# Kernel optimization log

Hardware: AMD Instinct MI355X
Metric: run time of the kernel (lower is better)

## Reference

```python
import jax, jax.numpy as jnp
import numpy as np

N_NODES = 50000
N_EDGES = 600000
D_IN = 128
D_OUT = 128
LN_EPS = 1e-5


def setup_inputs() -> dict:
    key = jax.random.key(0)
    ks = jax.random.split(key, 12)
    x = jax.random.normal(ks[0], (N_NODES, D_IN), dtype=jnp.float32)
    adj_in_rows = jax.random.randint(ks[1], (N_EDGES,), 0, N_NODES, dtype=jnp.int32)
    adj_in_cols = jax.random.randint(ks[2], (N_EDGES,), 0, N_NODES, dtype=jnp.int32)
    adj_in_vals = jax.random.uniform(ks[3], (N_EDGES,), dtype=jnp.float32)
    adj_out_rows = jax.random.randint(ks[4], (N_EDGES,), 0, N_NODES, dtype=jnp.int32)
    adj_out_cols = jax.random.randint(ks[5], (N_EDGES,), 0, N_NODES, dtype=jnp.int32)
    adj_out_vals = jax.random.uniform(ks[6], (N_EDGES,), dtype=jnp.float32)
    s = 1.0 / np.sqrt(D_IN)
    W_self = jax.random.uniform(ks[7], (D_OUT, D_IN), dtype=jnp.float32, minval=-s, maxval=s)
    b_self = jax.random.uniform(ks[8], (D_OUT,), dtype=jnp.float32, minval=-s, maxval=s)
    W_in = jax.random.uniform(ks[9], (D_OUT, D_IN), dtype=jnp.float32, minval=-s, maxval=s)
    W_out = jax.random.uniform(ks[10], (D_OUT, D_IN), dtype=jnp.float32, minval=-s, maxval=s)
    ln_gamma = jnp.ones((D_OUT,), dtype=jnp.float32)
    ln_beta = jnp.zeros((D_OUT,), dtype=jnp.float32)
    return {
        "x": x,
        "adj_in_rows": adj_in_rows, "adj_in_cols": adj_in_cols, "adj_in_vals": adj_in_vals,
        "adj_out_rows": adj_out_rows, "adj_out_cols": adj_out_cols, "adj_out_vals": adj_out_vals,
        "W_self": W_self, "b_self": b_self, "W_in": W_in, "W_out": W_out,
        "ln_gamma": ln_gamma, "ln_beta": ln_beta,
    }


def _spmm(rows, cols, vals, x, n):
    # COO sparse.mm: out[r] += vals[e] * x[cols[e]]
    return jax.ops.segment_sum(vals[:, None] * x[cols], rows, num_segments=n)


def reference(x, adj_in_rows, adj_in_cols, adj_in_vals,
              adj_out_rows, adj_out_cols, adj_out_vals,
              W_self, b_self, W_in, W_out, ln_gamma, ln_beta):
    n = x.shape[0]
    agg_in = _spmm(adj_in_rows, adj_in_cols, adj_in_vals, x, n)
    agg_out = _spmm(adj_out_rows, adj_out_cols, adj_out_vals, x, n)
    h = x @ W_self.T + b_self + agg_in @ W_in.T + agg_out @ W_out.T
    mu = jnp.mean(h, axis=-1, keepdims=True)
    var = jnp.mean(jnp.square(h - mu), axis=-1, keepdims=True)
    h = (h - mu) * jax.lax.rsqrt(var + LN_EPS) * ln_gamma + ln_beta
    # dropout is identity in eval mode (training=False)
    return jax.nn.relu(h)
```

## Files before the change

kernel.cpp:

```cpp
#include <hip/hip_runtime.h>

#define N_NODES 50000
#define N_EDGES 600000
#define D 128
#define BM 32
#define NT (2 * N_NODES)
#define NE2 (2 * N_EDGES)
#define NPAD 50048
#define KA 384
#define GBM 64
#define NB 1563
#define BROWS 64
#define CAPE 1024
#define CHUNK_A 8192

typedef __attribute__((ext_vector_type(8))) short bf16x8;
typedef __attribute__((ext_vector_type(4))) float f32x4;

__device__ inline unsigned short bfr(float x) {
    unsigned b = __float_as_uint(x);
    b += 0x7FFFu + ((b >> 16) & 1u);
    return (unsigned short)(b >> 16);
}
__device__ inline float bf_lo(unsigned u) { return __uint_as_float(u << 16); }
__device__ inline float bf_hi(unsigned u) { return __uint_as_float(u & 0xFFFF0000u); }


__global__ __launch_bounds__(256) void cvt_x(const float* __restrict__ x, short* __restrict__ A)
{
    int gid = blockIdx.x * 256 + threadIdx.x;
    if (gid >= N_NODES * 32) return;
    int row = gid >> 5, c4 = gid & 31;
    float4 v = *reinterpret_cast<const float4*>(x + (size_t)row * D + c4 * 4);
    ushort4 o = { bfr(v.x), bfr(v.y), bfr(v.z), bfr(v.w) };
    *reinterpret_cast<ushort4*>(A + (size_t)row * KA + c4 * 4) = o;
}

__global__ __launch_bounds__(384) void cvt_w(
    const float* __restrict__ Ws, const float* __restrict__ Wi,
    const float* __restrict__ Wo, short* __restrict__ Wc)
{
    int j = blockIdx.x, k = threadIdx.x;
    float v = (k < 128) ? Ws[j * 128 + k]
            : (k < 256) ? Wi[j * 128 + k - 128]
                        : Wo[j * 128 + k - 256];
    Wc[j * KA + k] = (short)bfr(v);
}


__global__ __launch_bounds__(1024) void bucket_hist(
    const int* __restrict__ ir, const int* __restrict__ orow, int* __restrict__ bcnt)
{
    __shared__ int h[NB];
    for (int i = threadIdx.x; i < NB; i += 1024) h[i] = 0;
    __syncthreads();
    int stride = gridDim.x * 1024;
    for (int e = blockIdx.x * 1024 + threadIdx.x; e < NE2; e += stride) {
        int r = (e < N_EDGES) ? ir[e] : N_NODES + orow[e - N_EDGES];
        atomicAdd(&h[r >> 6], 1);
    }
    __syncthreads();
    for (int i = threadIdx.x; i < NB; i += 1024)
        if (h[i]) atomicAdd(&bcnt[i], h[i]);
}

__global__ __launch_bounds__(1024) void scan_buckets(
    const int* __restrict__ bcnt, int* __restrict__ bbase, int* __restrict__ bcur)
{
    __shared__ int s[1024];
    const int t = threadIdx.x;
    const int i0 = 2 * t, i1 = 2 * t + 1;
    int v0 = (i0 < NB) ? bcnt[i0] : 0;
    int v1 = (i1 < NB) ? bcnt[i1] : 0;
    int v = v0 + v1;
    s[t] = v;
    __syncthreads();
    for (int o = 1; o < 1024; o <<= 1) {
        int u = (t >= o) ? s[t - o] : 0;
        __syncthreads();
        s[t] += u;
        __syncthreads();
    }
    int ex = s[t] - v;
    if (i0 < NB) { bbase[i0] = ex;      bcur[i0] = ex; }
    if (i1 < NB) { bbase[i1] = ex + v0; bcur[i1] = ex + v0; }
}

__global__ __launch_bounds__(1024) void scatter_buckets(
    const int* __restrict__ ir, const int* __restrict__ icol, const float* __restrict__ ival,
    const int* __restrict__ orow, const int* __restrict__ ocol, const float* __restrict__ oval,
    int* __restrict__ bcur, int2* __restrict__ pairp)
{
    __shared__ int2 pay[CHUNK_A];
    __shared__ int  dstp[CHUNK_A];
    __shared__ int  hist[NB];
    __shared__ int  lofs[NB];
    __shared__ int  gb2[NB];
    __shared__ int  sbuf[1024];

    const int t = threadIdx.x;
    for (int i = t; i < NB; i += 1024) hist[i] = 0;
    __syncthreads();

    const int e0 = blockIdx.x * CHUNK_A;
    const int m = min(NE2 - e0, CHUNK_A);
    int rr[8], cc[8]; float vv[8];
#pragma unroll
    for (int i = 0; i < 8; ++i) {
        int e = e0 + t + i * 1024;
        if (e < N_EDGES)      { rr[i] = ir[e];                       cc[i] = icol[e];           vv[i] = ival[e]; }
        else if (e < NE2)     { rr[i] = N_NODES + orow[e - N_EDGES]; cc[i] = ocol[e - N_EDGES]; vv[i] = oval[e - N_EDGES]; }
        else                  { rr[i] = -1; cc[i] = 0; vv[i] = 0.f; }
        if (rr[i] >= 0) atomicAdd(&hist[rr[i] >> 6], 1);
    }
    __syncthreads();

    const int i0 = 2 * t, i1 = 2 * t + 1;
    int h0 = (i0 < NB) ? hist[i0] : 0;
    int h1 = (i1 < NB) ? hist[i1] : 0;
    int hv = h0 + h1;
    sbuf[t] = hv;
    __syncthreads();
    for (int o = 1; o < 1024; o <<= 1) {
        int u = (t >= o) ? sbuf[t - o] : 0;
        __syncthreads();
        sbuf[t] += u;
        __syncthreads();
    }
    int ex = sbuf[t] - hv;
    if (i0 < NB) lofs[i0] = ex;
    if (i1 < NB) lofs[i1] = ex + h0;
    __syncthreads();

    for (int i = t; i < NB; i += 1024) {
        int c = hist[i];
        int g = c ? atomicAdd(&bcur[i], c) : 0;
        gb2[i] = g - lofs[i];
    }
    __syncthreads();
    for (int i = t; i < NB; i += 1024) hist[i] = lofs[i];
    __syncthreads();

#pragma unroll
    for (int i = 0; i < 8; ++i) {
        if (rr[i] < 0) continue;
        int bk = rr[i] >> 6;
        int s = atomicAdd(&hist[bk], 1);
        pay[s]  = make_int2((cc[i] & 0xFFFF) | ((rr[i] & 63) << 16), __float_as_int(vv[i]));
        dstp[s] = gb2[bk] + s;
    }
    __syncthreads();

    for (int i = t; i < m; i += 1024)
        pairp[dstp[i]] = pay[i];
}

__global__ __launch_bounds__(512) void bucket_spmm(
    const int* __restrict__ bbase, const int* __restrict__ bcnt,
    const int2* __restrict__ pairp, short* __restrict__ A)
{
    __shared__ int2 ed[CAPE];
    __shared__ int  rs[BROWS];
    __shared__ int  rstart[BROWS + 1];
    __shared__ int  rcur[BROWS];

    const int t = threadIdx.x;
    const int b = blockIdx.x;
    const int base = bbase[b];
    const int n = bcnt[b];
    const int w = t >> 6, lane = t & 63;
    const int h = lane >> 5, sl = lane & 31;
    const int row0 = w * 8;
    const char* Ab = (const char*)A + sl * 8;

    float4 acc[8];
#pragma unroll
    for (int i = 0; i < 8; ++i) acc[i] = make_float4(0.f, 0.f, 0.f, 0.f);

    for (int s0 = 0; s0 < n; s0 += CAPE) {
        const int m = min(n - s0, CAPE);
        if (t < BROWS) rs[t] = 0;
        __syncthreads();
        int2 myp[2];
#pragma unroll
        for (int k = 0; k < 2; ++k) {
            int i = t + k * 512;
            if (i < m) {
                myp[k] = pairp[base + s0 + i];
                atomicAdd(&rs[(myp[k].x >> 16) & 63], 1);
            }
        }
        __syncthreads();
        if (t < 64) {
            int v = rs[t];
            int a = v;
#pragma unroll
            for (int o = 1; o < 64; o <<= 1) {
                int u = __shfl_up(a, o);
                if (t >= o) a += u;
            }
            rstart[t] = a - v;
            rcur[t]   = a - v;
            if (t == 63) rstart[64] = a;
        }
        __syncthreads();
#pragma unroll
        for (int k = 0; k < 2; ++k) {
            int i = t + k * 512;
            if (i < m) {
                int pos = atomicAdd(&rcur[(myp[k].x >> 16) & 63], 1);
                ed[pos] = myp[k];
            }
        }
        __syncthreads();
#pragma unroll
        for (int ri = 0; ri < 8; ++ri) {
            const int r = row0 + ri;
            const int s = rstart[r], e2 = rstart[r + 1];
            float4 a = acc[ri];
            for (int i = s; i < e2; i += 8) {
#pragma unroll
                for (int k = 0; k < 4; ++k) {
                    int idx = i + 2 * k + h;
                    int2 p = ed[min(idx, e2 - 1)];
                    float v = (idx < e2) ? __int_as_float(p.y) : 0.f;
                    uint2 u = *(const uint2*)(Ab + (unsigned)((p.x & 0xFFFF) * (KA * 2)));
                    a.x += v * bf_lo(u.x);
                    a.y += v * bf_hi(u.x);
                    a.z += v * bf_lo(u.y);
                    a.w += v * bf_hi(u.y);
                }
            }
            acc[ri] = a;
        }
        __syncthreads();
    }

    char* Aw = (char*)A;
#pragma unroll
    for (int ri = 0; ri < 8; ++ri) {
        float4 a = acc[ri];
        a.x += __shfl_xor(a.x, 32);
        a.y += __shfl_xor(a.y, 32);
        a.z += __shfl_xor(a.z, 32);
        a.w += __shfl_xor(a.w, 32);
        int wv = b * BROWS + row0 + ri;
        if (lane < 32 && wv < NT) {
            uint2 o;
            o.x = ((unsigned)bfr(a.y) << 16) | (unsigned)bfr(a.x);
            o.y = ((unsigned)bfr(a.w) << 16) | (unsigned)bfr(a.z);
            size_t dst = (wv < N_NODES)
                       ? ((size_t)wv * (KA * 2) + 256 + sl * 8)
                       : ((size_t)(wv - N_NODES) * (KA * 2) + 512 + sl * 8);
            *(uint2*)(Aw + dst) = o;
        }
    }
}

__global__ __launch_bounds__(512) void gemm_mfma(
    const short* __restrict__ A, const short* __restrict__ Wc,
    const float* __restrict__ b, const float* __restrict__ gamma,
    const float* __restrict__ beta, float* __restrict__ out)
{
    __shared__ short Alds[GBM * KA];
    __shared__ float red[8][64][2];
    __shared__ float2 mustd[64];

    const int t = threadIdx.x;
    const int l = t & 63, w = t >> 6;
    const int q = l >> 4, c = l & 15;
    const int base = blockIdx.x * GBM;

    bf16x8 bfrag[12];
    const short* wrow = Wc + (size_t)(w * 16 + c) * KA + q * 8;
#pragma unroll
    for (int s = 0; s < 12; ++s)
        bfrag[s] = *reinterpret_cast<const bf16x8*>(wrow + s * 32);

#pragma unroll
    for (int i = 0; i < 6; ++i) {
        int slot = t + i * 512;
        int row = slot / 48, c16 = slot % 48;
        bf16x8 v = *reinterpret_cast<const bf16x8*>(A + (size_t)(base + row) * KA + c16 * 8);
        *reinterpret_cast<bf16x8*>(&Alds[row * KA + (c16 ^ (row & 7)) * 8]) = v;
    }
    __syncthreads();

    f32x4 acc[4];
#pragma unroll
    for (int rg = 0; rg < 4; ++rg) acc[rg] = (f32x4){0.f, 0.f, 0.f, 0.f};

#pragma unroll
    for (int s = 0; s < 12; ++s) {
#pragma unroll
        for (int rg = 0; rg < 4; ++rg) {
            int row = rg * 16 + c;
            int c16 = (s * 4 + q) ^ (row & 7);
            bf16x8 af = *reinterpret_cast<const bf16x8*>(&Alds[row * KA + c16 * 8]);
            acc[rg] = __builtin_amdgcn_mfma_f32_16x16x32_bf16(af, bfrag[s], acc[rg], 0, 0, 0);
        }
    }

    const float bj = b[w * 16 + c];
    const float gj = gamma[w * 16 + c];
    const float ej = beta[w * 16 + c];

#pragma unroll
    for (int rg = 0; rg < 4; ++rg) {
#pragma unroll
        for (int r = 0; r < 4; ++r) {
            float hv = acc[rg][r] + bj;
            acc[rg][r] = hv;
            float s1 = hv, s2 = hv * hv;
#pragma unroll
            for (int m = 1; m < 16; m <<= 1) {
                s1 += __shfl_xor(s1, m);
                s2 += __shfl_xor(s2, m);
            }
            if (c == 0) {
                int row = rg * 16 + q * 4 + r;
                red[w][row][0] = s1;
                red[w][row][1] = s2;
            }
        }
    }
    __syncthreads();

    if (t < 64) {
        float s1 = 0.f, s2 = 0.f;
#pragma unroll
        for (int ww = 0; ww < 8; ++ww) { s1 += red[ww][t][0]; s2 += red[ww][t][1]; }
        float mu = s1 * (1.f / 128.f);
        float var = s2 * (1.f / 128.f) - mu * mu;
        mustd[t] = make_float2(mu, rsqrtf(var + 1e-5f));
    }
    __syncthreads();

#pragma unroll
    for (int rg = 0; rg < 4; ++rg) {
        int row0 = rg * 16 + q * 4;
        int node0 = base + row0;
#pragma unroll
        for (int r = 0; r < 4; ++r) {
            float2 ms = mustd[row0 + r];
            float y = (acc[rg][r] - ms.x) * ms.y * gj + ej;
            y = fmaxf(y, 0.f);
            if (node0 + r < N_NODES)
                out[(size_t)(node0 + r) * D + w * 16 + c] = y;
        }
    }
}

__global__ __launch_bounds__(256) void spmm_scatter(
    const int* __restrict__ rows, const int* __restrict__ cols,
    const float* __restrict__ vals, const float* __restrict__ x,
    float* __restrict__ agg, int nE)
{
    int g = blockIdx.x * 256 + threadIdx.x;
    int e = g >> 5;
    if (e >= nE) return;
    int q = g & 31;
    int r = rows[e], c = cols[e];
    float v = vals[e];
    float4 xv = *reinterpret_cast<const float4*>(x + (size_t)c * D + (size_t)q * 4);
    float* ap = agg + (size_t)r * D + (size_t)q * 4;
    atomicAdd(ap + 0, v * xv.x);
    atomicAdd(ap + 1, v * xv.y);
    atomicAdd(ap + 2, v * xv.z);
    atomicAdd(ap + 3, v * xv.w);
}

__global__ __launch_bounds__(256) void gemm_ln_relu(
    const float* __restrict__ x, const float* __restrict__ agg_in,
    const float* __restrict__ agg_out,
    const float* __restrict__ Ws, const float* __restrict__ Wi,
    const float* __restrict__ Wo, const float* __restrict__ b,
    const float* __restrict__ gamma, const float* __restrict__ beta,
    float* __restrict__ out, int n)
{
    __shared__ float4 Wl[D * (D / 4)];
    __shared__ float4 Xl[BM * (D / 4)];

    const int t = threadIdx.x;
    const int l = t & 63;
    const int w = t >> 6;
    const int base = blockIdx.x * BM;
    const int j0 = l, j1 = l + 64;

    float acc0[8], acc1[8];
    const float bj0 = b[j0], bj1 = b[j1];
#pragma unroll
    for (int i = 0; i < 8; ++i) { acc0[i] = bj0; acc1[i] = bj1; }

    const float* srcs[3] = { x, agg_in, agg_out };
    const float* wms[3]  = { Ws, Wi, Wo };

#pragma unroll
    for (int s = 0; s < 3; ++s) {
        const float4* src4 = reinterpret_cast<const float4*>(srcs[s]);
        const float4* w4   = reinterpret_cast<const float4*>(wms[s]);
        __syncthreads();
#pragma unroll
        for (int it = 0; it < 16; ++it) {
            int gi = t + 256 * it;
            int j = gi >> 5, k4 = gi & 31;
            Wl[j * 32 + (k4 ^ (j & 7))] = w4[gi];
        }
#pragma unroll
        for (int it = 0; it < 4; ++it) {
            int gi = t + 256 * it;
            int m = gi >> 5, k4 = gi & 31;
            int node = base + m;
            float4 v = (node < n) ? src4[(size_t)node * 32 + k4]
                                  : make_float4(0.f, 0.f, 0.f, 0.f);
            Xl[m * 32 + k4] = v;
        }
        __syncthreads();

        const int sw = j0 & 7;
#pragma unroll 8
        for (int k4 = 0; k4 < 32; ++k4) {
            float4 w0 = Wl[j0 * 32 + (k4 ^ sw)];
            float4 w1 = Wl[j1 * 32 + (k4 ^ sw)];
#pragma unroll
            for (int i = 0; i < 8; ++i) {
                float4 xv = Xl[(w + 4 * i) * 32 + k4];
                acc0[i] += xv.x * w0.x + xv.y * w0.y + xv.z * w0.z + xv.w * w0.w;
                acc1[i] += xv.x * w1.x + xv.y * w1.y + xv.z * w1.z + xv.w * w1.w;
            }
        }
    }

    const float g0 = gamma[j0], g1 = gamma[j1];
    const float be0 = beta[j0], be1 = beta[j1];
#pragma unroll
    for (int i = 0; i < 8; ++i) {
        int node = base + w + 4 * i;
        float s  = acc0[i] + acc1[i];
        float ss = acc0[i] * acc0[i] + acc1[i] * acc1[i];
#pragma unroll
        for (int off = 32; off; off >>= 1) {
            s  += __shfl_xor(s, off);
            ss += __shfl_xor(ss, off);
        }
        float mu   = s * (1.0f / D);
        float var  = ss * (1.0f / D) - mu * mu;
        float rstd = rsqrtf(var + 1e-5f);
        if (node < n) {
            float y0 = (acc0[i] - mu) * rstd * g0 + be0;
            float y1 = (acc1[i] - mu) * rstd * g1 + be1;
            out[(size_t)node * D + j0] = fmaxf(y0, 0.f);
            out[(size_t)node * D + j1] = fmaxf(y1, 0.f);
        }
    }
}

extern "C" void kernel_launch(void* const* d_in, const int* in_sizes, int n_in,
                              void* d_out, int out_size, void* d_ws, size_t ws_size,
                              hipStream_t stream) {
    const float* x     = (const float*)d_in[0];
    const int*   ir    = (const int*)  d_in[1];
    const int*   icoln = (const int*)  d_in[2];
    const float* ival  = (const float*)d_in[3];
    const int*   orow  = (const int*)  d_in[4];
    const int*   ocol  = (const int*)  d_in[5];
    const float* oval  = (const float*)d_in[6];
    const float* Ws    = (const float*)d_in[7];
    const float* b     = (const float*)d_in[8];
    const float* Wi    = (const float*)d_in[9];
    const float* Wo    = (const float*)d_in[10];
    const float* gamma = (const float*)d_in[11];
    const float* beta  = (const float*)d_in[12];
    float* out = (float*)d_out;

    short* A     = (short*)d_ws;
    short* Wc    = A + (size_t)NPAD * KA;
    int*   bcnt  = (int*)(Wc + (size_t)128 * KA);
    int*   bbase = bcnt + NB;
    int*   bcur  = bbase + NB;
    int2*  pairp = (int2*)(bcur + NB + ((3 * NB) & 1));
    size_t need  = (size_t)NPAD * KA * 2 + (size_t)128 * KA * 2
                 + (size_t)(3 * NB + 2) * 4 + (size_t)NE2 * 8;

    if (ws_size >= need) {
        hipMemsetAsync(bcnt, 0, NB * sizeof(int), stream);
        hipMemsetAsync(A + (size_t)N_NODES * KA, 0,
                       (size_t)(NPAD - N_NODES) * KA * 2, stream);

        cvt_x<<<(N_NODES * 32 + 255) / 256, 256, 0, stream>>>(x, A);
        cvt_w<<<128, 384, 0, stream>>>(Ws, Wi, Wo, Wc);

        bucket_hist<<<128, 1024, 0, stream>>>(ir, orow, bcnt);
        scan_buckets<<<1, 1024, 0, stream>>>(bcnt, bbase, bcur);
        scatter_buckets<<<(NE2 + CHUNK_A - 1) / CHUNK_A, 1024, 0, stream>>>(
            ir, icoln, ival, orow, ocol, oval, bcur, pairp);
        bucket_spmm<<<NB, 512, 0, stream>>>(bbase, bcnt, pairp, A);

        gemm_mfma<<<NPAD / GBM, 512, 0, stream>>>(A, Wc, b, gamma, beta, out);
    } else {
        float* agg_in  = (float*)d_ws;
        float* agg_out = agg_in + (size_t)N_NODES * D;
        hipMemsetAsync(d_ws, 0, 2 * (size_t)N_NODES * D * sizeof(float), stream);
        const int eblocks = (N_EDGES * 32 + 255) / 256;
        spmm_scatter<<<eblocks, 256, 0, stream>>>(ir, icoln, ival, x, agg_in, N_EDGES);
        spmm_scatter<<<eblocks, 256, 0, stream>>>(orow, ocol, oval, x, agg_out, N_EDGES);
        const int gblocks = (N_NODES + BM - 1) / BM;
        gemm_ln_relu<<<gblocks, 256, 0, stream>>>(x, agg_in, agg_out, Ws, Wi, Wo,
                                                  b, gamma, beta, out, N_NODES);
    }
}
```

Measured before the change: 137.9 us.

## Fuse bucketed SpMM aggregation into MFMA GEMM with per-node buckets

```diff
diff --git a/kernel.cpp b/kernel.cpp
--- a/kernel.cpp
+++ b/kernel.cpp
@@ -8,9 +8,8 @@
 #define NE2 (2 * N_EDGES)
 #define NPAD 50048
 #define KA 384
-#define GBM 64
-#define NB 1563
-#define BROWS 64
+#define NBK 782
+#define VR 128
 #define CAPE 1024
 #define CHUNK_A 8192
 
@@ -26,14 +25,14 @@
 __device__ inline float bf_hi(unsigned u) { return __uint_as_float(u & 0xFFFF0000u); }
 
 
-__global__ __launch_bounds__(256) void cvt_x(const float* __restrict__ x, short* __restrict__ A)
+__global__ __launch_bounds__(256) void cvt_x(const float* __restrict__ x, short* __restrict__ Xb)
 {
     int gid = blockIdx.x * 256 + threadIdx.x;
     if (gid >= N_NODES * 32) return;
     int row = gid >> 5, c4 = gid & 31;
     float4 v = *reinterpret_cast<const float4*>(x + (size_t)row * D + c4 * 4);
     ushort4 o = { bfr(v.x), bfr(v.y), bfr(v.z), bfr(v.w) };
-    *reinterpret_cast<ushort4*>(A + (size_t)row * KA + c4 * 4) = o;
+    *reinterpret_cast<ushort4*>(Xb + (size_t)row * D + c4 * 4) = o;
 }
 
 __global__ __launch_bounds__(384) void cvt_w(
@@ -51,16 +50,16 @@
 __global__ __launch_bounds__(1024) void bucket_hist(
     const int* __restrict__ ir, const int* __restrict__ orow, int* __restrict__ bcnt)
 {
-    __shared__ int h[NB];
-    for (int i = threadIdx.x; i < NB; i += 1024) h[i] = 0;
+    __shared__ int h[NBK];
+    for (int i = threadIdx.x; i < NBK; i += 1024) h[i] = 0;
     __syncthreads();
     int stride = gridDim.x * 1024;
     for (int e = blockIdx.x * 1024 + threadIdx.x; e < NE2; e += stride) {
-        int r = (e < N_EDGES) ? ir[e] : N_NODES + orow[e - N_EDGES];
-        atomicAdd(&h[r >> 6], 1);
-    }
-    __syncthreads();
-    for (int i = threadIdx.x; i < NB; i += 1024)
+        int node = (e < N_EDGES) ? ir[e] : orow[e - N_EDGES];
+        atomicAdd(&h[node >> 6], 1);
+    }
+    __syncthreads();
+    for (int i = threadIdx.x; i < NBK; i += 1024)
         if (h[i]) atomicAdd(&bcnt[i], h[i]);
 }
 
@@ -69,10 +68,7 @@
 {
     __shared__ int s[1024];
     const int t = threadIdx.x;
-    const int i0 = 2 * t, i1 = 2 * t + 1;
-    int v0 = (i0 < NB) ? bcnt[i0] : 0;
-    int v1 = (i1 < NB) ? bcnt[i1] : 0;
-    int v = v0 + v1;
+    int v = (t < NBK) ? bcnt[t] : 0;
     s[t] = v;
     __syncthreads();
     for (int o = 1; o < 1024; o <<= 1) {
@@ -81,9 +77,7 @@
         s[t] += u;
         __syncthreads();
     }
-    int ex = s[t] - v;
-    if (i0 < NB) { bbase[i0] = ex;      bcur[i0] = ex; }
-    if (i1 < NB) { bbase[i1] = ex + v0; bcur[i1] = ex + v0; }
+    if (t < NBK) { bbase[t] = s[t] - v; bcur[t] = s[t] - v; }
 }
 
 __global__ __launch_bounds__(1024) void scatter_buckets(
@@ -93,32 +87,35 @@
 {
     __shared__ int2 pay[CHUNK_A];
     __shared__ int  dstp[CHUNK_A];
-    __shared__ int  hist[NB];
-    __shared__ int  lofs[NB];
-    __shared__ int  gb2[NB];
+    __shared__ int  hist[NBK];
+    __shared__ int  lofs[NBK];
+    __shared__ int  gb2[NBK];
     __shared__ int  sbuf[1024];
 
     const int t = threadIdx.x;
-    for (int i = t; i < NB; i += 1024) hist[i] = 0;
+    for (int i = t; i < NBK; i += 1024) hist[i] = 0;
     __syncthreads();
 
     const int e0 = blockIdx.x * CHUNK_A;
     const int m = min(NE2 - e0, CHUNK_A);
-    int rr[8], cc[8]; float vv[8];
+    int bk8[8], px[8], vv[8];
 #pragma unroll
     for (int i = 0; i < 8; ++i) {
         int e = e0 + t + i * 1024;
-        if (e < N_EDGES)      { rr[i] = ir[e];                       cc[i] = icol[e];           vv[i] = ival[e]; }
-        else if (e < NE2)     { rr[i] = N_NODES + orow[e - N_EDGES]; cc[i] = ocol[e - N_EDGES]; vv[i] = oval[e - N_EDGES]; }
-        else                  { rr[i] = -1; cc[i] = 0; vv[i] = 0.f; }
-        if (rr[i] >= 0) atomicAdd(&hist[rr[i] >> 6], 1);
-    }
-    __syncthreads();
-
-    const int i0 = 2 * t, i1 = 2 * t + 1;
-    int h0 = (i0 < NB) ? hist[i0] : 0;
-    int h1 = (i1 < NB) ? hist[i1] : 0;
-    int hv = h0 + h1;
+        int node, col, flag; float val;
+        if (e < N_EDGES)      { node = ir[e];            col = icol[e];            val = ival[e];            flag = 0; }
+        else if (e < NE2)     { node = orow[e - N_EDGES]; col = ocol[e - N_EDGES]; val = oval[e - N_EDGES];  flag = 64; }
+        else                  { node = -1; col = 0; val = 0.f; flag = 0; }
+        if (node >= 0) {
+            bk8[i] = node >> 6;
+            px[i]  = (col & 0xFFFF) | (((node & 63) | flag) << 16);
+            vv[i]  = __float_as_int(val);
+            atomicAdd(&hist[bk8[i]], 1);
+        } else bk8[i] = -1;
+    }
+    __syncthreads();
+
+    int hv = (t < NBK) ? hist[t] : 0;
     sbuf[t] = hv;
     __syncthreads();
     for (int o = 1; o < 1024; o <<= 1) {
@@ -127,27 +124,24 @@
         sbuf[t] += u;
         __syncthreads();
     }
-    int ex = sbuf[t] - hv;
-    if (i0 < NB) lofs[i0] = ex;
-    if (i1 < NB) lofs[i1] = ex + h0;
-    __syncthreads();
-
-    for (int i = t; i < NB; i += 1024) {
+    if (t < NBK) lofs[t] = sbuf[t] - hv;
+    __syncthreads();
+
+    for (int i = t; i < NBK; i += 1024) {
         int c = hist[i];
         int g = c ? atomicAdd(&bcur[i], c) : 0;
         gb2[i] = g - lofs[i];
     }
     __syncthreads();
-    for (int i = t; i < NB; i += 1024) hist[i] = lofs[i];
+    for (int i = t; i < NBK; i += 1024) hist[i] = lofs[i];
     __syncthreads();
 
 #pragma unroll
     for (int i = 0; i < 8; ++i) {
-        if (rr[i] < 0) continue;
-        int bk = rr[i] >> 6;
-        int s = atomicAdd(&hist[bk], 1);
-        pay[s]  = make_int2((cc[i] & 0xFFFF) | ((rr[i] & 63) << 16), __float_as_int(vv[i]));
-        dstp[s] = gb2[bk] + s;
+        if (bk8[i] < 0) continue;
+        int s = atomicAdd(&hist[bk8[i]], 1);
+        pay[s]  = make_int2(px[i], vv[i]);
+        dstp[s] = gb2[bk8[i]] + s;
     }
     __syncthreads();
 
@@ -155,31 +149,46 @@
         pairp[dstp[i]] = pay[i];
 }
 
-__global__ __launch_bounds__(512) void bucket_spmm(
+__global__ __launch_bounds__(512, 4) void spmm_gemm(
     const int* __restrict__ bbase, const int* __restrict__ bcnt,
-    const int2* __restrict__ pairp, short* __restrict__ A)
-{
-    __shared__ int2 ed[CAPE];
-    __shared__ int  rs[BROWS];
-    __shared__ int  rstart[BROWS + 1];
-    __shared__ int  rcur[BROWS];
+    const int2* __restrict__ pairp, const short* __restrict__ Xb,
+    const short* __restrict__ Wc, const float* __restrict__ b,
+    const float* __restrict__ gamma, const float* __restrict__ beta,
+    float* __restrict__ out)
+{
+    __shared__ short Alds[64 * KA];
+    __shared__ int2  ed[CAPE];
+    __shared__ int   rs[VR];
+    __shared__ int   rstart[VR + 1];
+    __shared__ int   rcur[VR];
+    __shared__ float red[8][64][2];
+    __shared__ float2 mustd[64];
 
     const int t = threadIdx.x;
-    const int b = blockIdx.x;
-    const int base = bbase[b];
-    const int n = bcnt[b];
-    const int w = t >> 6, lane = t & 63;
+    const int bk = blockIdx.x;
+    const int lane = t & 63, w = t >> 6;
     const int h = lane >> 5, sl = lane & 31;
-    const int row0 = w * 8;
-    const char* Ab = (const char*)A + sl * 8;
-
-    float4 acc[8];
-#pragma unroll
-    for (int i = 0; i < 8; ++i) acc[i] = make_float4(0.f, 0.f, 0.f, 0.f);
+    const int nodebase = bk * 64;
+
+#pragma unroll
+    for (int i = 0; i < 2; ++i) {
+        int slot = t + i * 512;
+        int row = slot >> 4, c16 = slot & 15;
+        bf16x8 v = *reinterpret_cast<const bf16x8*>(Xb + (size_t)(nodebase + row) * D + c16 * 8);
+        *reinterpret_cast<bf16x8*>(&Alds[row * KA + (c16 ^ (row & 7)) * 8]) = v;
+    }
+
+    const int base = bbase[bk];
+    const int n = bcnt[bk];
+    const char* Ab = (const char*)Xb + sl * 8;
+
+    float4 acc[16];
+#pragma unroll
+    for (int i = 0; i < 16; ++i) acc[i] = make_float4(0.f, 0.f, 0.f, 0.f);
 
     for (int s0 = 0; s0 < n; s0 += CAPE) {
         const int m = min(n - s0, CAPE);
-        if (t < BROWS) rs[t] = 0;
+        if (t < VR) rs[t] = 0;
         __syncthreads();
         int2 myp[2];
 #pragma unroll
@@ -187,44 +196,45 @@
             int i = t + k * 512;
             if (i < m) {
                 myp[k] = pairp[base + s0 + i];
-                atomicAdd(&rs[(myp[k].x >> 16) & 63], 1);
+                atomicAdd(&rs[(myp[k].x >> 16) & 127], 1);
             }
         }
         __syncthreads();
         if (t < 64) {
-            int v = rs[t];
-            int a = v;
+            int v0 = rs[2 * t], v1 = rs[2 * t + 1];
+            int v = v0 + v1, a = v;
 #pragma unroll
             for (int o = 1; o < 64; o <<= 1) {
                 int u = __shfl_up(a, o);
                 if (t >= o) a += u;
             }
-            rstart[t] = a - v;
-            rcur[t]   = a - v;
-            if (t == 63) rstart[64] = a;
+            int ex = a - v;
+            rstart[2 * t] = ex;          rcur[2 * t] = ex;
+            rstart[2 * t + 1] = ex + v0; rcur[2 * t + 1] = ex + v0;
+            if (t == 63) rstart[VR] = a;
         }
         __syncthreads();
 #pragma unroll
         for (int k = 0; k < 2; ++k) {
             int i = t + k * 512;
             if (i < m) {
-                int pos = atomicAdd(&rcur[(myp[k].x >> 16) & 63], 1);
+                int pos = atomicAdd(&rcur[(myp[k].x >> 16) & 127], 1);
                 ed[pos] = myp[k];
             }
         }
         __syncthreads();
 #pragma unroll
-        for (int ri = 0; ri < 8; ++ri) {
-            const int r = row0 + ri;
+        for (int ri = 0; ri < 16; ++ri) {
+            const int r = w * 16 + ri;
             const int s = rstart[r], e2 = rstart[r + 1];
             float4 a = acc[ri];
-            for (int i = s; i < e2; i += 8) {
-#pragma unroll
-                for (int k = 0; k < 4; ++k) {
+            for (int i = s; i < e2; i += 16) {
+#pragma unroll
+                for (int k = 0; k < 8; ++k) {
                     int idx = i + 2 * k + h;
                     int2 p = ed[min(idx, e2 - 1)];
                     float v = (idx < e2) ? __int_as_float(p.y) : 0.f;
-                    uint2 u = *(const uint2*)(Ab + (unsigned)((p.x & 0xFFFF) * (KA * 2)));
+                    uint2 u = *(const uint2*)(Ab + (unsigned)((p.x & 0xFFFF) * (D * 2)));
                     a.x += v * bf_lo(u.x);
                     a.y += v * bf_hi(u.x);
                     a.z += v * bf_lo(u.y);
@@ -236,68 +246,60 @@
         __syncthreads();
     }
 
-    char* Aw = (char*)A;
-#pragma unroll
-    for (int ri = 0; ri < 8; ++ri) {
+#pragma unroll
+    for (int ri = 0; ri < 16; ++ri) {
         float4 a = acc[ri];
         a.x += __shfl_xor(a.x, 32);
         a.y += __shfl_xor(a.y, 32);
         a.z += __shfl_xor(a.z, 32);
         a.w += __shfl_xor(a.w, 32);
-        int wv = b * BROWS + row0 + ri;
-        if (lane < 32 && wv < NT) {
+        if (lane < 32) {
+            int vrow = w * 16 + ri;
+            int row = vrow & 63;
+            int flag = vrow >> 6;
+            int c16 = 16 + flag * 16 + (sl >> 1);
             uint2 o;
             o.x = ((unsigned)bfr(a.y) << 16) | (unsigned)bfr(a.x);
             o.y = ((unsigned)bfr(a.w) << 16) | (unsigned)bfr(a.z);
-            size_t dst = (wv < N_NODES)
-                       ? ((size_t)wv * (KA * 2) + 256 + sl * 8)
-                       : ((size_t)(wv - N_NODES) * (KA * 2) + 512 + sl * 8);
-            *(uint2*)(Aw + dst) = o;
-        }
-    }
-}
-
-__global__ __launch_bounds__(512) void gemm_mfma(
-    const short* __restrict__ A, const short* __restrict__ Wc,
-    const float* __restrict__ b, const float* __restrict__ gamma,
-    const float* __restrict__ beta, float* __restrict__ out)
-{
-    __shared__ short Alds[GBM * KA];
-    __shared__ float red[8][64][2];
-    __shared__ float2 mustd[64];
-
-    const int t = threadIdx.x;
-    const int l = t & 63, w = t >> 6;
-    const int q = l >> 4, c = l & 15;
-    const int base = blockIdx.x * GBM;
-
-    bf16x8 bfrag[12];
+            char* dst = (char*)Alds + row * (KA * 2) + (c16 ^ (row & 7)) * 16 + (sl & 1) * 8;
+            *(uint2*)dst = o;
+        }
+    }
+
+    const int q = lane >> 4, c = lane & 15;
     const short* wrow = Wc + (size_t)(w * 16 + c) * KA + q * 8;
-#pragma unroll
-    for (int s = 0; s < 12; ++s)
+
+    bf16x8 bfrag[6];
+#pragma unroll
+    for (int s = 0; s < 6; ++s)
         bfrag[s] = *reinterpret_cast<const bf16x8*>(wrow + s * 32);
-
-#pragma unroll
-    for (int i = 0; i < 6; ++i) {
-        int slot = t + i * 512;
-        int row = slot / 48, c16 = slot % 48;
-        bf16x8 v = *reinterpret_cast<const bf16x8*>(A + (size_t)(base + row) * KA + c16 * 8);
-        *reinterpret_cast<bf16x8*>(&Alds[row * KA + (c16 ^ (row & 7)) * 8]) = v;
-    }
-    __syncthreads();
-
-    f32x4 acc[4];
-#pragma unroll
-    for (int rg = 0; rg < 4; ++rg) acc[rg] = (f32x4){0.f, 0.f, 0.f, 0.f};
-
-#pragma unroll
-    for (int s = 0; s < 12; ++s) {
+    __syncthreads();
+
+    f32x4 acg[4];
+#pragma unroll
+    for (int rg = 0; rg < 4; ++rg) acg[rg] = (f32x4){0.f, 0.f, 0.f, 0.f};
+
+#pragma unroll
+    for (int s = 0; s < 6; ++s) {
 #pragma unroll
         for (int rg = 0; rg < 4; ++rg) {
             int row = rg * 16 + c;
             int c16 = (s * 4 + q) ^ (row & 7);
             bf16x8 af = *reinterpret_cast<const bf16x8*>(&Alds[row * KA + c16 * 8]);
-            acc[rg] = __builtin_amdgcn_mfma_f32_16x16x32_bf16(af, bfrag[s], acc[rg], 0, 0, 0);
+            acg[rg] = __builtin_amdgcn_mfma_f32_16x16x32_bf16(af, bfrag[s], acg[rg], 0, 0, 0);
+        }
+    }
+#pragma unroll
+    for (int s = 0; s < 6; ++s)
+        bfrag[s] = *reinterpret_cast<const bf16x8*>(wrow + (s + 6) * 32);
+#pragma unroll
+    for (int s = 0; s < 6; ++s) {
+#pragma unroll
+        for (int rg = 0; rg < 4; ++rg) {
+            int row = rg * 16 + c;
+            int c16 = ((s + 6) * 4 + q) ^ (row & 7);
+            bf16x8 af = *reinterpret_cast<const bf16x8*>(&Alds[row * KA + c16 * 8]);
+            acg[rg] = __builtin_amdgcn_mfma_f32_16x16x32_bf16(af, bfrag[s], acg[rg], 0, 0, 0);
         }
     }
 
@@ -309,13 +311,13 @@
     for (int rg = 0; rg < 4; ++rg) {
 #pragma unroll
         for (int r = 0; r < 4; ++r) {
-            float hv = acc[rg][r] + bj;
-            acc[rg][r] = hv;
+            float hv = acg[rg][r] + bj;
+            acg[rg][r] = hv;
             float s1 = hv, s2 = hv * hv;
 #pragma unroll
-            for (int m = 1; m < 16; m <<= 1) {
-                s1 += __shfl_xor(s1, m);
-                s2 += __shfl_xor(s2, m);
+            for (int m2 = 1; m2 < 16; m2 <<= 1) {
+                s1 += __shfl_xor(s1, m2);
+                s2 += __shfl_xor(s2, m2);
             }
             if (c == 0) {
                 int row = rg * 16 + q * 4 + r;
@@ -339,11 +341,11 @@
 #pragma unroll
     for (int rg = 0; rg < 4; ++rg) {
         int row0 = rg * 16 + q * 4;
-        int node0 = base + row0;
+        int node0 = nodebase + row0;
 #pragma unroll
         for (int r = 0; r < 4; ++r) {
             float2 ms = mustd[row0 + r];
-            float y = (acc[rg][r] - ms.x) * ms.y * gj + ej;
+            float y = (acg[rg][r] - ms.x) * ms.y * gj + ej;
             y = fmaxf(y, 0.f);
             if (node0 + r < N_NODES)
                 out[(size_t)(node0 + r) * D + w * 16 + c] = y;
@@ -473,30 +475,30 @@
     const float* beta  = (const float*)d_in[12];
     float* out = (float*)d_out;
 
-    short* A     = (short*)d_ws;
-    short* Wc    = A + (size_t)NPAD * KA;
+    short* Xb    = (short*)d_ws;
+    short* Wc    = Xb + (size_t)NPAD * D;
     int*   bcnt  = (int*)(Wc + (size_t)128 * KA);
-    int*   bbase = bcnt + NB;
-    int*   bcur  = bbase + NB;
-    int2*  pairp = (int2*)(bcur + NB + ((3 * NB) & 1));
-    size_t need  = (size_t)NPAD * KA * 2 + (size_t)128 * KA * 2
-                 + (size_t)(3 * NB + 2) * 4 + (size_t)NE2 * 8;
+    int*   bbase = bcnt + NBK;
+    int*   bcur  = bbase + NBK;
+    int2*  pairp = (int2*)(bcur + NBK + ((3 * NBK) & 1));
+    size_t need  = (size_t)NPAD * D * 2 + (size_t)128 * KA * 2
+                 + (size_t)(3 * NBK + 2) * 4 + (size_t)NE2 * 8;
 
     if (ws_size >= need) {
-        hipMemsetAsync(bcnt, 0, NB * sizeof(int), stream);
-        hipMemsetAsync(A + (size_t)N_NODES * KA, 0,
-                       (size_t)(NPAD - N_NODES) * KA * 2, stream);
-
-        cvt_x<<<(N_NODES * 32 + 255) / 256, 256, 0, stream>>>(x, A);
+        hipMemsetAsync(bcnt, 0, NBK * sizeof(int), stream);
+        hipMemsetAsync(Xb + (size_t)N_NODES * D, 0,
+                       (size_t)(NPAD - N_NODES) * D * 2, stream);
+
+        cvt_x<<<(N_NODES * 32 + 255) / 256, 256, 0, stream>>>(x, Xb);
         cvt_w<<<128, 384, 0, stream>>>(Ws, Wi, Wo, Wc);
 
         bucket_hist<<<128, 1024, 0, stream>>>(ir, orow, bcnt);
         scan_buckets<<<1, 1024, 0, stream>>>(bcnt, bbase, bcur);
         scatter_buckets<<<(NE2 + CHUNK_A - 1) / CHUNK_A, 1024, 0, stream>>>(
             ir, icoln, ival, orow, ocol, oval, bcur, pairp);
-        bucket_spmm<<<NB, 512, 0, stream>>>(bbase, bcnt, pairp, A);
-
-        gemm_mfma<<<NPAD / GBM, 512, 0, stream>>>(A, Wc, b, gamma, beta, out);
+
+        spmm_gemm<<<NBK, 512, 0, stream>>>(bbase, bcnt, pairp, Xb, Wc,
+                                           b, gamma, beta, out);
     } else {
         float* agg_in  = (float*)d_ws;
         float* agg_out = agg_in + (size_t)N_NODES * D;
```

After: 163.2 us. 18.4% more time.
